# Performance work log

Measured on AMD Instinct MI355X. Metric: run time of the kernel, lower is better.

Reference implementation:

```python
import jax, jax.numpy as jnp
import numpy as np

B, N, D = 4, 2048, 512   # batch, seq, feed_forward_size
H, DK, DV = 8, 64, 64    # heads, key_dim, value_dim
LN_EPS = 1e-5


def setup_inputs() -> dict:
    key = jax.random.key(0)
    ks = jax.random.split(key, 12)
    s = 0.02
    x = jax.random.normal(ks[0], (B, N, D), dtype=jnp.float32)
    # boolean mask, True = masked out (torch masked_fill semantics); causal
    attn_mask = ~jnp.tril(jnp.ones((N, N), dtype=bool))[None, None]
    ln_g = jnp.ones((D,), jnp.float32)
    ln_b = jnp.zeros((D,), jnp.float32)
    wq = jax.random.normal(ks[1], (D, H * DK), jnp.float32) * s
    bq = jnp.zeros((H * DK,), jnp.float32)
    wk = jax.random.normal(ks[2], (D, H * DK), jnp.float32) * s
    bk = jnp.zeros((H * DK,), jnp.float32)
    wv = jax.random.normal(ks[3], (D, H * DV), jnp.float32) * s
    bv = jnp.zeros((H * DV,), jnp.float32)
    wo = jax.random.normal(ks[4], (H * DV, D), jnp.float32) * s
    bo = jnp.zeros((D,), jnp.float32)
    return {"x": x, "attn_mask": attn_mask, "ln_g": ln_g, "ln_b": ln_b,
            "wq": wq, "bq": bq, "wk": wk, "bk": bk, "wv": wv, "bv": bv,
            "wo": wo, "bo": bo}


def _layernorm(x, g, b):
    mu = jnp.mean(x, axis=-1, keepdims=True)
    var = jnp.mean(jnp.square(x - mu), axis=-1, keepdims=True)
    return (x - mu) * jax.lax.rsqrt(var + LN_EPS) * g + b


def reference(x, attn_mask, ln_g, ln_b, wq, bq, wk, bk, wv, bv, wo, bo):
    xn = _layernorm(x, ln_g, ln_b)
    scale = DK ** -0.5
    q = (xn @ wq + bq).reshape(B, N, H, DK).transpose(0, 2, 1, 3) * scale  # b h n d
    k = (xn @ wk + bk).reshape(B, N, H, DK).transpose(0, 2, 1, 3)
    v = (xn @ wv + bv).reshape(B, N, H, DV).transpose(0, 2, 1, 3)
    sim = jnp.einsum('bhid,bhjd->bhij', q, k)
    sim = jnp.where(attn_mask, -jnp.finfo(sim.dtype).max, sim)
    attn = jax.nn.softmax(sim, axis=-1)  # dropout p=0 (eval)
    out = jnp.einsum('bhij,bhjd->bhid', attn, v)
    out = out.transpose(0, 2, 1, 3).reshape(B, N, H * DV)  # b n (h d)
    return out @ wo + bo
```

## Files before the change

kernel.cpp:

```cpp
#include <hip/hip_runtime.h>

typedef unsigned short u16;
typedef unsigned long long u64;
typedef __bf16 bf16x8 __attribute__((ext_vector_type(8)));
typedef float f32x4 __attribute__((ext_vector_type(4)));
typedef float f32x16 __attribute__((ext_vector_type(16)));

#define H_HEADS 8
#define DHEAD 64
#define NSEQ 2048
#define DMODEL 512
#define BATCH 4
#define MROWS (BATCH * NSEQ)
#define BH (BATCH * H_HEADS)

__device__ __forceinline__ u16 f2bf(float f) {
  unsigned u = __builtin_bit_cast(unsigned, f);
  u += 0x7fffu + ((u >> 16) & 1u);
  return (u16)(u >> 16);
}

__device__ __forceinline__ float bf2f(u16 v) {
  unsigned u = (unsigned)v << 16;
  return __builtin_bit_cast(float, u);
}

__device__ __forceinline__ bf16x8 ldfrag(const u16* p) {
  return __builtin_bit_cast(bf16x8, *(const uint4*)p);
}

typedef __attribute__((address_space(1))) void GV;
typedef __attribute__((address_space(3))) void LV;
__device__ __forceinline__ void gld16(const void* g, void* l) {
  __builtin_amdgcn_global_load_lds((GV*)g, (LV*)l, 16, 0, 0);
}

__global__ __launch_bounds__(256) void ln_w_kernel(
    const float* __restrict__ x, const float* __restrict__ g,
    const float* __restrict__ b, u16* __restrict__ xn,
    const float* __restrict__ w0, const float* __restrict__ w1,
    const float* __restrict__ w2, const float* __restrict__ w3,
    u16* __restrict__ WT) {
  __shared__ float tile[32][33];
  const int t = threadIdx.x;
  if (blockIdx.x < MROWS) {
    const int row = blockIdx.x;
    const float2 v = *(const float2*)(x + (size_t)row * DMODEL + t * 2);
    float s = v.x + v.y;
    float ss = v.x * v.x + v.y * v.y;
    #pragma unroll
    for (int d = 1; d < 64; d <<= 1) {
      s += __shfl_xor(s, d);
      ss += __shfl_xor(ss, d);
    }
    const int wave = t >> 6, lane = t & 63;
    if (lane == 0) { tile[0][wave] = s; tile[0][4 + wave] = ss; }
    __syncthreads();
    s = tile[0][0] + tile[0][1] + tile[0][2] + tile[0][3];
    ss = tile[0][4] + tile[0][5] + tile[0][6] + tile[0][7];
    const float mean = s * (1.0f / DMODEL);
    const float var = ss * (1.0f / DMODEL) - mean * mean;
    const float rstd = rsqrtf(var + 1e-5f);
    const float2 gg = *(const float2*)(g + t * 2);
    const float2 bb = *(const float2*)(b + t * 2);
    const float o0 = (v.x - mean) * rstd * gg.x + bb.x;
    const float o1 = (v.y - mean) * rstd * gg.y + bb.y;
    const unsigned packed = (unsigned)f2bf(o0) | ((unsigned)f2bf(o1) << 16);
    *(unsigned*)(xn + (size_t)row * DMODEL + t * 2) = packed;
  } else {
    const int u = blockIdx.x - MROWS;
    const int z = u >> 8;
    const int rem = u & 255;
    const float* W = (z == 0) ? w0 : (z == 1) ? w1 : (z == 2) ? w2 : w3;
    u16* dst = WT + (size_t)z * DMODEL * DMODEL;
    const int n0 = (rem & 15) * 32, k0 = (rem >> 4) * 32;
    #pragma unroll
    for (int p = 0; p < 4; ++p) {
      const int uu = p * 256 + t;
      const int r = uu >> 5, c = uu & 31;
      tile[r][c] = W[(size_t)(k0 + r) * DMODEL + n0 + c];
    }
    __syncthreads();
    #pragma unroll
    for (int p = 0; p < 4; ++p) {
      const int uu = p * 256 + t;
      const int rn = uu >> 5, ck = uu & 31;
      dst[(size_t)(n0 + rn) * DMODEL + k0 + ck] = f2bf(tile[ck][rn]);
    }
  }
}

template <int MODE>
__global__ __launch_bounds__(512) void gemm128_kernel(
    const u16* __restrict__ A, const u16* __restrict__ BT,
    const float* __restrict__ bq, const float* __restrict__ bk,
    const float* __restrict__ bv,
    u16* __restrict__ qb, u16* __restrict__ kb, u16* __restrict__ vtb,
    float* __restrict__ fout, int K) {
  __shared__ u16 lds_a[128 * 64];
  __shared__ u16 lds_b[128 * 64];
  const int t = threadIdx.x;
  const int lane = t & 63, wave = t >> 6;
  const int wm = wave >> 2, wn = wave & 3;
  const int lo = lane & 15, hi = lane >> 4;
  const int nwg = gridDim.x * gridDim.y;
  const int lid = blockIdx.y * gridDim.x + blockIdx.x;
  const int sid = (lid & 7) * (nwg >> 3) + (lid >> 3);
  const int m0 = (sid / gridDim.x) * 128, n0 = (sid % gridDim.x) * 128;
  const int sr = lane >> 3;
  const int scol = (((lane & 7) ^ sr) * 8);
  f32x4 acc[4][2] = {};
  for (int k0 = 0; k0 < K; k0 += 64) {
    #pragma unroll
    for (int j = 0; j < 2; ++j) {
      const int ch = wave * 2 + j;
      gld16(A + (size_t)(m0 + ch * 8 + sr) * K + k0 + scol, lds_a + ch * 512);
      gld16(BT + (size_t)(n0 + ch * 8 + sr) * K + k0 + scol, lds_b + ch * 512);
    }
    __syncthreads();
    #pragma unroll
    for (int kc = 0; kc < 2; ++kc) {
      bf16x8 af[4], bfr[2];
      const int sw = ((lo & 7) * 8);
      #pragma unroll
      for (int i = 0; i < 4; ++i)
        af[i] = ldfrag(lds_a + (wm * 64 + i * 16 + lo) * 64 + ((kc * 32 + hi * 8) ^ sw));
      #pragma unroll
      for (int i = 0; i < 2; ++i)
        bfr[i] = ldfrag(lds_b + (wn * 32 + i * 16 + lo) * 64 + ((kc * 32 + hi * 8) ^ sw));
      __builtin_amdgcn_s_setprio(1);
      #pragma unroll
      for (int mi = 0; mi < 4; ++mi)
        #pragma unroll
        for (int ni = 0; ni < 2; ++ni)
          acc[mi][ni] = __builtin_amdgcn_mfma_f32_16x16x32_bf16(
              af[mi], bfr[ni], acc[mi][ni], 0, 0, 0);
      __builtin_amdgcn_s_setprio(0);
    }
    __syncthreads();
  }
  #pragma unroll
  for (int mi = 0; mi < 4; ++mi) {
    #pragma unroll
    for (int ni = 0; ni < 2; ++ni) {
      const int col = n0 + wn * 32 + ni * 16 + lo;
      if (MODE == 0) {
        const int mat = col >> 9, w = col & 511;
        const int hh = w >> 6, dk = w & 63;
        const float bi = (mat == 0 ? bq : (mat == 1 ? bk : bv))[w];
        const int row0 = m0 + wm * 64 + mi * 16 + hi * 4;
        const int bbx = row0 >> 11, seq0 = row0 & 2047;
        if (mat == 2) {
          u64 pk = 0;
          #pragma unroll
          for (int r = 0; r < 4; ++r)
            pk |= (u64)f2bf(acc[mi][ni][r] + bi) << (16 * r);
          *(u64*)(vtb + ((size_t)(bbx * H_HEADS + hh) * DHEAD + dk) * NSEQ + seq0) = pk;
        } else {
          const float sc = (mat == 0) ? 0.18033688f : 1.0f;
          u16* dst = (mat == 0 ? qb : kb);
          #pragma unroll
          for (int r = 0; r < 4; ++r)
            dst[(((size_t)(bbx * H_HEADS + hh) * NSEQ) + seq0 + r) * DHEAD + dk] =
                f2bf((acc[mi][ni][r] + bi) * sc);
        }
      } else {
        const float bi = bq[col];
        #pragma unroll
        for (int r = 0; r < 4; ++r) {
          const int row = m0 + wm * 64 + mi * 16 + hi * 4 + r;
          fout[(size_t)row * DMODEL + col] = acc[mi][ni][r] + bi;
        }
      }
    }
  }
}

__global__ __launch_bounds__(256, 4) void attn_kernel(
    const u16* __restrict__ Q, const u16* __restrict__ K,
    const u16* __restrict__ VT, u16* __restrict__ O,
    u16* __restrict__ pO, float* __restrict__ pL) {
  __shared__ u16 lds_k[2][4096];
  __shared__ u16 lds_v[2][4096];
  const int t = threadIdx.x;
  const int lane = t & 63, wave = t >> 6;
  const int l31 = lane & 31, hi = lane >> 5;
  const int l7 = lane & 7;

  const int nraw = blockIdx.x;
  const int n = (nraw & 7) * 160 + (nraw >> 3);
  const int bh = n / 40;
  const int r = n % 40;
  int qt, ck, C;
  if (r < 4)       { qt = r;                 C = 1; ck = 0; }
  else if (r < 12) { qt = 4 + ((r - 4) >> 1);  C = 2; ck = (r - 4) & 1; }
  else if (r < 24) { qt = 8 + (r - 12) / 3;    C = 3; ck = (r - 12) % 3; }
  else             { qt = 12 + ((r - 24) >> 2); C = 4; ck = (r - 24) & 3; }
  const int T = 2 * qt + 2;
  const int kc0 = (ck * T) / C;
  const int L = ((ck + 1) * T) / C - kc0;

  const int b = bh >> 3, h = bh & 7;
  const u16* Qh = Q + (size_t)bh * NSEQ * DHEAD;
  const u16* Kh = K + (size_t)bh * NSEQ * DHEAD;
  const u16* Vh = VT + (size_t)bh * DHEAD * NSEQ;

  const int q0w = qt * 128 + wave * 32;
  const int lastkt = (q0w + 31) >> 6;
  const int qrow = q0w + l31;

  bf16x8 qf[4];
  #pragma unroll
  for (int c = 0; c < 4; ++c)
    qf[c] = ldfrag(Qh + (size_t)qrow * DHEAD + c * 16 + hi * 8);

  f32x16 o0 = {}, o1 = {};
  float l = 0.0f;

  const int sr = lane >> 3;
  const int scol = ((lane & 7) ^ sr) * 8;
  const int swz = l7 * 8;

  #pragma unroll
  for (int j = 0; j < 2; ++j) {
    const int ch = wave * 2 + j;
    gld16(Kh + (size_t)(kc0 * 64 + ch * 8 + sr) * DHEAD + scol, lds_k[0] + ch * 512);
    gld16(Vh + (size_t)(ch * 8 + sr) * NSEQ + kc0 * 64 + scol, lds_v[0] + ch * 512);
  }

  for (int lt = 0; lt < L; ++lt) {
    const int gk = kc0 + lt;
    const int cur = lt & 1;
    if (lt + 1 < L) {
      const int kvn = (gk + 1) * 64;
      #pragma unroll
      for (int j = 0; j < 2; ++j) {
        const int ch = wave * 2 + j;
        gld16(Kh + (size_t)(kvn + ch * 8 + sr) * DHEAD + scol, lds_k[cur ^ 1] + ch * 512);
        gld16(Vh + (size_t)(ch * 8 + sr) * NSEQ + kvn + scol, lds_v[cur ^ 1] + ch * 512);
      }
      asm volatile("s_waitcnt vmcnt(4)" ::: "memory");
    } else {
      asm volatile("s_waitcnt vmcnt(0)" ::: "memory");
    }
    __builtin_amdgcn_s_barrier();
    __builtin_amdgcn_sched_barrier(0);

    if (gk <= lastkt) {
      const u16* lk = lds_k[cur];
      const u16* lv = lds_v[cur];
      f32x16 st0 = {}, st1 = {};

      __builtin_amdgcn_s_setprio(1);
      #pragma unroll
      for (int c = 0; c < 4; ++c) {
        const int col = (c * 16 + hi * 8) ^ swz;
        bf16x8 kf0 = ldfrag(lk + l31 * 64 + col);
        bf16x8 kf1 = ldfrag(lk + (32 + l31) * 64 + col);
        st0 = __builtin_amdgcn_mfma_f32_32x32x16_bf16(kf0, qf[c], st0, 0, 0, 0);
        st1 = __builtin_amdgcn_mfma_f32_32x32x16_bf16(kf1, qf[c], st1, 0, 0, 0);
      }
      __builtin_amdgcn_s_setprio(0);

      if (gk == lastkt) {
        const int kvb = gk * 64 + 4 * hi;
        #pragma unroll
        for (int rr = 0; rr < 16; ++rr) {
          const int kv = kvb + (rr & 3) + 8 * (rr >> 2);
          if (kv > qrow) st0[rr] = -1e30f;
          if (kv + 32 > qrow) st1[rr] = -1e30f;
        }
      }

      #pragma unroll
      for (int rr = 0; rr < 16; ++rr) st0[rr] = exp2f(st0[rr]);
      #pragma unroll
      for (int rr = 0; rr < 16; ++rr) st1[rr] = exp2f(st1[rr]);
      float sm[16];
      #pragma unroll
      for (int i = 0; i < 16; ++i) sm[i] = st0[i] + st1[i];
      #pragma unroll
      for (int stp = 8; stp; stp >>= 1)
        #pragma unroll
        for (int i = 0; i < stp; ++i) sm[i] += sm[i + stp];
      l += sm[0];

      bf16x8 pf0, pf1, pf2, pf3;
      {
        unsigned w0, w1, w2, w3, w4, w5, w6, w7;
        asm("v_cvt_pk_bf16_f32 %0, %1, %2" : "=v"(w0) : "v"(st0[0]), "v"(st0[1]));
        asm("v_cvt_pk_bf16_f32 %0, %1, %2" : "=v"(w1) : "v"(st0[2]), "v"(st0[3]));
        asm("v_cvt_pk_bf16_f32 %0, %1, %2" : "=v"(w2) : "v"(st0[4]), "v"(st0[5]));
        asm("v_cvt_pk_bf16_f32 %0, %1, %2" : "=v"(w3) : "v"(st0[6]), "v"(st0[7]));
        asm("v_cvt_pk_bf16_f32 %0, %1, %2" : "=v"(w4) : "v"(st0[8]), "v"(st0[9]));
        asm("v_cvt_pk_bf16_f32 %0, %1, %2" : "=v"(w5) : "v"(st0[10]), "v"(st0[11]));
        asm("v_cvt_pk_bf16_f32 %0, %1, %2" : "=v"(w6) : "v"(st0[12]), "v"(st0[13]));
        asm("v_cvt_pk_bf16_f32 %0, %1, %2" : "=v"(w7) : "v"(st0[14]), "v"(st0[15]));
        asm("v_permlane32_swap_b32 %0, %1" : "+v"(w0), "+v"(w2));
        asm("v_permlane32_swap_b32 %0, %1" : "+v"(w1), "+v"(w3));
        asm("v_permlane32_swap_b32 %0, %1" : "+v"(w4), "+v"(w6));
        asm("v_permlane32_swap_b32 %0, %1" : "+v"(w5), "+v"(w7));
        union Uu { unsigned u[4]; bf16x8 v; };
        Uu a; a.u[0] = w0; a.u[1] = w1; a.u[2] = w2; a.u[3] = w3; pf0 = a.v;
        Uu bb; bb.u[0] = w4; bb.u[1] = w5; bb.u[2] = w6; bb.u[3] = w7; pf1 = bb.v;
      }
      {
        unsigned w0, w1, w2, w3, w4, w5, w6, w7;
        asm("v_cvt_pk_bf16_f32 %0, %1, %2" : "=v"(w0) : "v"(st1[0]), "v"(st1[1]));
        asm("v_cvt_pk_bf16_f32 %0, %1, %2" : "=v"(w1) : "v"(st1[2]), "v"(st1[3]));
        asm("v_cvt_pk_bf16_f32 %0, %1, %2" : "=v"(w2) : "v"(st1[4]), "v"(st1[5]));
        asm("v_cvt_pk_bf16_f32 %0, %1, %2" : "=v"(w3) : "v"(st1[6]), "v"(st1[7]));
        asm("v_cvt_pk_bf16_f32 %0, %1, %2" : "=v"(w4) : "v"(st1[8]), "v"(st1[9]));
        asm("v_cvt_pk_bf16_f32 %0, %1, %2" : "=v"(w5) : "v"(st1[10]), "v"(st1[11]));
        asm("v_cvt_pk_bf16_f32 %0, %1, %2" : "=v"(w6) : "v"(st1[12]), "v"(st1[13]));
        asm("v_cvt_pk_bf16_f32 %0, %1, %2" : "=v"(w7) : "v"(st1[14]), "v"(st1[15]));
        asm("v_permlane32_swap_b32 %0, %1" : "+v"(w0), "+v"(w2));
        asm("v_permlane32_swap_b32 %0, %1" : "+v"(w1), "+v"(w3));
        asm("v_permlane32_swap_b32 %0, %1" : "+v"(w4), "+v"(w6));
        asm("v_permlane32_swap_b32 %0, %1" : "+v"(w5), "+v"(w7));
        union Uu { unsigned u[4]; bf16x8 v; };
        Uu a; a.u[0] = w0; a.u[1] = w1; a.u[2] = w2; a.u[3] = w3; pf2 = a.v;
        Uu bb; bb.u[0] = w4; bb.u[1] = w5; bb.u[2] = w6; bb.u[3] = w7; pf3 = bb.v;
      }

      __builtin_amdgcn_s_setprio(1);
      #pragma unroll
      for (int c = 0; c < 4; ++c) {
        const int col = (c * 16 + hi * 8) ^ swz;
        bf16x8 vf0 = ldfrag(lv + l31 * 64 + col);
        bf16x8 vf1 = ldfrag(lv + (32 + l31) * 64 + col);
        const bf16x8 pc = (c == 0) ? pf0 : (c == 1) ? pf1 : (c == 2) ? pf2 : pf3;
        o0 = __builtin_amdgcn_mfma_f32_32x32x16_bf16(vf0, pc, o0, 0, 0, 0);
        o1 = __builtin_amdgcn_mfma_f32_32x32x16_bf16(vf1, pc, o1, 0, 0, 0);
      }
      __builtin_amdgcn_s_setprio(0);
    }
    __builtin_amdgcn_sched_barrier(0);
    __builtin_amdgcn_s_barrier();
    __builtin_amdgcn_sched_barrier(0);
  }

  l += __shfl_xor(l, 32);

  if (C == 1) {
    const float rl = __builtin_amdgcn_rcpf(l);
    u16* Ob = O + ((size_t)b * NSEQ + qrow) * DMODEL + h * DHEAD;
    #pragma unroll
    for (int d = 0; d < 2; ++d) {
      #pragma unroll
      for (int mq = 0; mq < 4; ++mq) {
        u64 pk = 0;
        #pragma unroll
        for (int c3 = 0; c3 < 4; ++c3) {
          const float v = (d ? o1[mq * 4 + c3] : o0[mq * 4 + c3]) * rl;
          pk |= (u64)f2bf(v) << (16 * c3);
        }
        *(u64*)(Ob + d * 32 + mq * 8 + hi * 4) = pk;
      }
    }
  } else {
    const int rloc = wave * 32 + l31;
    u16* po = pO + (size_t)n * (128 * 64) + (size_t)rloc * 64;
    #pragma unroll
    for (int d = 0; d < 2; ++d) {
      #pragma unroll
      for (int mq = 0; mq < 4; ++mq) {
        u64 pk = 0;
        #pragma unroll
        for (int c3 = 0; c3 < 4; ++c3) {
          const float v = d ? o1[mq * 4 + c3] : o0[mq * 4 + c3];
          pk |= (u64)f2bf(v) << (16 * c3);
        }
        *(u64*)(po + d * 32 + mq * 8 + hi * 4) = pk;
      }
    }
    if (hi == 0) pL[(size_t)n * 128 + rloc] = l;
  }
}

__global__ __launch_bounds__(256) void attn_merge_kernel(
    const u16* __restrict__ pO, const float* __restrict__ pL,
    u16* __restrict__ O) {
  const int u = blockIdx.x;
  const int bh = u / 12, qi = u % 12;
  const int qt = 4 + qi;
  const int C = (qt >> 2) + 1;
  int off;
  if (qt < 8) off = 4 + 2 * (qt - 4);
  else if (qt < 12) off = 12 + 3 * (qt - 8);
  else off = 24 + 4 * (qt - 12);
  const int slot0 = bh * 40 + off;
  const int t = threadIdx.x;
  const int row = t >> 1, db = (t & 1) * 32;

  float ls = 0.0f;
  float a[32];
  #pragma unroll
  for (int k = 0; k < 32; ++k) a[k] = 0.0f;
  #pragma unroll
  for (int c = 0; c < 4; ++c) {
    if (c < C) {
      ls += pL[(size_t)(slot0 + c) * 128 + row];
      const u16* src = pO + (size_t)(slot0 + c) * (128 * 64) + (size_t)row * 64 + db;
      #pragma unroll
      for (int q4 = 0; q4 < 4; ++q4) {
        const uint4 v = *(const uint4*)(src + q4 * 8);
        const unsigned uu[4] = {v.x, v.y, v.z, v.w};
        #pragma unroll
        for (int j = 0; j < 4; ++j) {
          a[q4 * 8 + j * 2]     += bf2f((u16)(uu[j] & 0xffff));
          a[q4 * 8 + j * 2 + 1] += bf2f((u16)(uu[j] >> 16));
        }
      }
    }
  }
  const float rl = __builtin_amdgcn_rcpf(ls);
  const int b = bh >> 3, h = bh & 7;
  u16* dst = O + ((size_t)b * NSEQ + qt * 128 + row) * DMODEL + h * DHEAD + db;
  #pragma unroll
  for (int k4 = 0; k4 < 8; ++k4) {
    u64 pk = 0;
    #pragma unroll
    for (int j = 0; j < 4; ++j)
      pk |= (u64)f2bf(a[k4 * 4 + j] * rl) << (16 * j);
    *(u64*)(dst + k4 * 4) = pk;
  }
}

extern "C" void kernel_launch(void* const* d_in, const int* in_sizes, int n_in,
                              void* d_out, int out_size, void* d_ws, size_t ws_size,
                              hipStream_t stream) {
  const float* x = (const float*)d_in[0];
  const float* ln_g = (const float*)d_in[2];
  const float* ln_b = (const float*)d_in[3];
  const float* wq = (const float*)d_in[4];
  const float* bq = (const float*)d_in[5];
  const float* wk = (const float*)d_in[6];
  const float* bk = (const float*)d_in[7];
  const float* wv = (const float*)d_in[8];
  const float* bv = (const float*)d_in[9];
  const float* wo = (const float*)d_in[10];
  const float* bo = (const float*)d_in[11];

  char* ws = (char*)d_ws;
  u16* xn = (u16*)ws;     ws += (size_t)MROWS * DMODEL * 2;
  u16* wqkvT = (u16*)ws;  ws += (size_t)4 * DMODEL * DMODEL * 2;
  u16* woT = wqkvT + (size_t)3 * DMODEL * DMODEL;
  u16* qb = (u16*)ws;     ws += (size_t)MROWS * DMODEL * 2;
  u16* kb = (u16*)ws;     ws += (size_t)MROWS * DMODEL * 2;
  u16* vtb = (u16*)ws;    ws += (size_t)MROWS * DMODEL * 2;
  u16* attnb = (u16*)ws;  ws += (size_t)MROWS * DMODEL * 2;
  u16* pO = (u16*)ws;     ws += (size_t)1280 * 128 * 64 * 2;
  float* pL = (float*)ws; ws += (size_t)1280 * 128 * 4;

  ln_w_kernel<<<MROWS + 1024, 256, 0, stream>>>(
      x, ln_g, ln_b, xn, wq, wk, wv, wo, wqkvT);

  gemm128_kernel<0><<<dim3(12, 64), 512, 0, stream>>>(
      xn, wqkvT, bq, bk, bv, qb, kb, vtb, nullptr, DMODEL);

  attn_kernel<<<1280, 256, 0, stream>>>(qb, kb, vtb, attnb, pO, pL);
  attn_merge_kernel<<<384, 256, 0, stream>>>(pO, pL, attnb);

  gemm128_kernel<1><<<dim3(4, 64), 512, 0, stream>>>(
      attnb, woT, bo, nullptr, nullptr, nullptr, nullptr, nullptr,
      (float*)d_out, DMODEL);
}
```

Before: 95.64 us.

## Fuse split-KV attention merge into output projection GEMM A-tile load

The separate attention merge kernel and the attention output buffer are removed. The output-projection GEMM now builds its A tile by summing the split partial outputs, normalizing by the summed row sums, and writing bf16 into LDS. Every attention block, including single-chunk ones, now writes partials instead of the final output. This drops one launch and a full round trip of the attention output through global memory. In exchange, the merge work is repeated across the four N-tile blocks, and the A load becomes synchronous register loads instead of async global-to-LDS copies.

```diff
diff --git a/kernel.cpp b/kernel.cpp
--- a/kernel.cpp
+++ b/kernel.cpp
@@ -33,6 +33,13 @@
 typedef __attribute__((address_space(3))) void LV;
 __device__ __forceinline__ void gld16(const void* g, void* l) {
   __builtin_amdgcn_global_load_lds((GV*)g, (LV*)l, 16, 0, 0);
+}
+
+__device__ __forceinline__ int qt_off(int qt) {
+  if (qt < 4) return qt;
+  if (qt < 8) return 4 + 2 * (qt - 4);
+  if (qt < 12) return 12 + 3 * (qt - 8);
+  return 24 + 4 * (qt - 12);
 }
 
 __global__ __launch_bounds__(256) void ln_w_kernel(
@@ -90,32 +97,30 @@
   }
 }
 
-template <int MODE>
-__global__ __launch_bounds__(512) void gemm128_kernel(
+__global__ __launch_bounds__(512) void gemm_qkv_kernel(
     const u16* __restrict__ A, const u16* __restrict__ BT,
     const float* __restrict__ bq, const float* __restrict__ bk,
     const float* __restrict__ bv,
-    u16* __restrict__ qb, u16* __restrict__ kb, u16* __restrict__ vtb,
-    float* __restrict__ fout, int K) {
+    u16* __restrict__ qb, u16* __restrict__ kb, u16* __restrict__ vtb) {
   __shared__ u16 lds_a[128 * 64];
   __shared__ u16 lds_b[128 * 64];
   const int t = threadIdx.x;
   const int lane = t & 63, wave = t >> 6;
   const int wm = wave >> 2, wn = wave & 3;
   const int lo = lane & 15, hi = lane >> 4;
-  const int nwg = gridDim.x * gridDim.y;
-  const int lid = blockIdx.y * gridDim.x + blockIdx.x;
+  const int nwg = 12 * 64;
+  const int lid = blockIdx.y * 12 + blockIdx.x;
   const int sid = (lid & 7) * (nwg >> 3) + (lid >> 3);
-  const int m0 = (sid / gridDim.x) * 128, n0 = (sid % gridDim.x) * 128;
+  const int m0 = (sid / 12) * 128, n0 = (sid % 12) * 128;
   const int sr = lane >> 3;
   const int scol = (((lane & 7) ^ sr) * 8);
   f32x4 acc[4][2] = {};
-  for (int k0 = 0; k0 < K; k0 += 64) {
+  for (int k0 = 0; k0 < DMODEL; k0 += 64) {
     #pragma unroll
     for (int j = 0; j < 2; ++j) {
       const int ch = wave * 2 + j;
-      gld16(A + (size_t)(m0 + ch * 8 + sr) * K + k0 + scol, lds_a + ch * 512);
-      gld16(BT + (size_t)(n0 + ch * 8 + sr) * K + k0 + scol, lds_b + ch * 512);
+      gld16(A + (size_t)(m0 + ch * 8 + sr) * DMODEL + k0 + scol, lds_a + ch * 512);
+      gld16(BT + (size_t)(n0 + ch * 8 + sr) * DMODEL + k0 + scol, lds_b + ch * 512);
     }
     __syncthreads();
     #pragma unroll
@@ -144,33 +149,24 @@
     #pragma unroll
     for (int ni = 0; ni < 2; ++ni) {
       const int col = n0 + wn * 32 + ni * 16 + lo;
-      if (MODE == 0) {
-        const int mat = col >> 9, w = col & 511;
-        const int hh = w >> 6, dk = w & 63;
-        const float bi = (mat == 0 ? bq : (mat == 1 ? bk : bv))[w];
-        const int row0 = m0 + wm * 64 + mi * 16 + hi * 4;
-        const int bbx = row0 >> 11, seq0 = row0 & 2047;
-        if (mat == 2) {
-          u64 pk = 0;
-          #pragma unroll
-          for (int r = 0; r < 4; ++r)
-            pk |= (u64)f2bf(acc[mi][ni][r] + bi) << (16 * r);
-          *(u64*)(vtb + ((size_t)(bbx * H_HEADS + hh) * DHEAD + dk) * NSEQ + seq0) = pk;
-        } else {
-          const float sc = (mat == 0) ? 0.18033688f : 1.0f;
-          u16* dst = (mat == 0 ? qb : kb);
-          #pragma unroll
-          for (int r = 0; r < 4; ++r)
-            dst[(((size_t)(bbx * H_HEADS + hh) * NSEQ) + seq0 + r) * DHEAD + dk] =
-                f2bf((acc[mi][ni][r] + bi) * sc);
-        }
+      const int mat = col >> 9, w = col & 511;
+      const int hh = w >> 6, dk = w & 63;
+      const float bi = (mat == 0 ? bq : (mat == 1 ? bk : bv))[w];
+      const int row0 = m0 + wm * 64 + mi * 16 + hi * 4;
+      const int bbx = row0 >> 11, seq0 = row0 & 2047;
+      if (mat == 2) {
+        u64 pk = 0;
+        #pragma unroll
+        for (int r = 0; r < 4; ++r)
+          pk |= (u64)f2bf(acc[mi][ni][r] + bi) << (16 * r);
+        *(u64*)(vtb + ((size_t)(bbx * H_HEADS + hh) * DHEAD + dk) * NSEQ + seq0) = pk;
       } else {
-        const float bi = bq[col];
-        #pragma unroll
-        for (int r = 0; r < 4; ++r) {
-          const int row = m0 + wm * 64 + mi * 16 + hi * 4 + r;
-          fout[(size_t)row * DMODEL + col] = acc[mi][ni][r] + bi;
-        }
+        const float sc = (mat == 0) ? 0.18033688f : 1.0f;
+        u16* dst = (mat == 0 ? qb : kb);
+        #pragma unroll
+        for (int r = 0; r < 4; ++r)
+          dst[(((size_t)(bbx * H_HEADS + hh) * NSEQ) + seq0 + r) * DHEAD + dk] =
+              f2bf((acc[mi][ni][r] + bi) * sc);
       }
     }
   }
@@ -178,7 +174,7 @@
 
 __global__ __launch_bounds__(256, 4) void attn_kernel(
     const u16* __restrict__ Q, const u16* __restrict__ K,
-    const u16* __restrict__ VT, u16* __restrict__ O,
+    const u16* __restrict__ VT,
     u16* __restrict__ pO, float* __restrict__ pL) {
   __shared__ u16 lds_k[2][4096];
   __shared__ u16 lds_v[2][4096];
@@ -200,7 +196,6 @@
   const int kc0 = (ck * T) / C;
   const int L = ((ck + 1) * T) / C - kc0;
 
-  const int b = bh >> 3, h = bh & 7;
   const u16* Qh = Q + (size_t)bh * NSEQ * DHEAD;
   const u16* Kh = K + (size_t)bh * NSEQ * DHEAD;
   const u16* Vh = VT + (size_t)bh * DHEAD * NSEQ;
@@ -342,88 +337,111 @@
 
   l += __shfl_xor(l, 32);
 
-  if (C == 1) {
-    const float rl = __builtin_amdgcn_rcpf(l);
-    u16* Ob = O + ((size_t)b * NSEQ + qrow) * DMODEL + h * DHEAD;
-    #pragma unroll
-    for (int d = 0; d < 2; ++d) {
-      #pragma unroll
-      for (int mq = 0; mq < 4; ++mq) {
-        u64 pk = 0;
-        #pragma unroll
-        for (int c3 = 0; c3 < 4; ++c3) {
-          const float v = (d ? o1[mq * 4 + c3] : o0[mq * 4 + c3]) * rl;
-          pk |= (u64)f2bf(v) << (16 * c3);
-        }
-        *(u64*)(Ob + d * 32 + mq * 8 + hi * 4) = pk;
-      }
-    }
-  } else {
-    const int rloc = wave * 32 + l31;
-    u16* po = pO + (size_t)n * (128 * 64) + (size_t)rloc * 64;
-    #pragma unroll
-    for (int d = 0; d < 2; ++d) {
-      #pragma unroll
-      for (int mq = 0; mq < 4; ++mq) {
-        u64 pk = 0;
-        #pragma unroll
-        for (int c3 = 0; c3 < 4; ++c3) {
-          const float v = d ? o1[mq * 4 + c3] : o0[mq * 4 + c3];
-          pk |= (u64)f2bf(v) << (16 * c3);
-        }
-        *(u64*)(po + d * 32 + mq * 8 + hi * 4) = pk;
-      }
-    }
-    if (hi == 0) pL[(size_t)n * 128 + rloc] = l;
-  }
-}
-
-__global__ __launch_bounds__(256) void attn_merge_kernel(
+  const int rloc = wave * 32 + l31;
+  u16* po = pO + (size_t)n * (128 * 64) + (size_t)rloc * 64;
+  #pragma unroll
+  for (int d = 0; d < 2; ++d) {
+    #pragma unroll
+    for (int mq = 0; mq < 4; ++mq) {
+      u64 pk = 0;
+      #pragma unroll
+      for (int c3 = 0; c3 < 4; ++c3) {
+        const float v = d ? o1[mq * 4 + c3] : o0[mq * 4 + c3];
+        pk |= (u64)f2bf(v) << (16 * c3);
+      }
+      *(u64*)(po + d * 32 + mq * 8 + hi * 4) = pk;
+    }
+  }
+  if (hi == 0) pL[(size_t)n * 128 + rloc] = l;
+}
+
+__global__ __launch_bounds__(512) void gemm_out_kernel(
     const u16* __restrict__ pO, const float* __restrict__ pL,
-    u16* __restrict__ O) {
-  const int u = blockIdx.x;
-  const int bh = u / 12, qi = u % 12;
-  const int qt = 4 + qi;
+    const u16* __restrict__ BT, const float* __restrict__ bo,
+    float* __restrict__ fout) {
+  __shared__ u16 lds_a[128 * 64];
+  __shared__ u16 lds_b[128 * 64];
+  const int t = threadIdx.x;
+  const int lane = t & 63, wave = t >> 6;
+  const int wm = wave >> 2, wn = wave & 3;
+  const int lo = lane & 15, hi = lane >> 4;
+  const int nwg = 4 * 64;
+  const int lid = blockIdx.y * 4 + blockIdx.x;
+  const int sid = (lid & 7) * (nwg >> 3) + (lid >> 3);
+  const int m0 = (sid >> 2) * 128, n0 = (sid & 3) * 128;
+  const int sr = lane >> 3;
+  const int l7 = lane & 7;
+  const int scol = ((l7 ^ sr) * 8);
+
+  const int bq = m0 >> 11;
+  const int qt = (m0 & 2047) >> 7;
   const int C = (qt >> 2) + 1;
-  int off;
-  if (qt < 8) off = 4 + 2 * (qt - 4);
-  else if (qt < 12) off = 12 + 3 * (qt - 8);
-  else off = 24 + 4 * (qt - 12);
-  const int slot0 = bh * 40 + off;
-  const int t = threadIdx.x;
-  const int row = t >> 1, db = (t & 1) * 32;
-
-  float ls = 0.0f;
-  float a[32];
+  const int off = qt_off(qt);
+
+  f32x4 acc[4][2] = {};
+  for (int k0 = 0; k0 < DMODEL; k0 += 64) {
+    const int h = k0 >> 6;
+    const int slot0 = (bq * H_HEADS + h) * 40 + off;
+    #pragma unroll
+    for (int j = 0; j < 2; ++j) {
+      const int ch = wave * 2 + j;
+      const int row = ch * 8 + sr;
+      float ls = 0.0f;
+      float av[8] = {0.f, 0.f, 0.f, 0.f, 0.f, 0.f, 0.f, 0.f};
+      for (int c = 0; c < C; ++c) {
+        ls += pL[(size_t)(slot0 + c) * 128 + row];
+        const uint4 v = *(const uint4*)(pO + (size_t)(slot0 + c) * 8192 +
+                                        (size_t)row * 64 + l7 * 8);
+        const unsigned uu0 = v.x, uu1 = v.y, uu2 = v.z, uu3 = v.w;
+        av[0] += bf2f((u16)(uu0 & 0xffff)); av[1] += bf2f((u16)(uu0 >> 16));
+        av[2] += bf2f((u16)(uu1 & 0xffff)); av[3] += bf2f((u16)(uu1 >> 16));
+        av[4] += bf2f((u16)(uu2 & 0xffff)); av[5] += bf2f((u16)(uu2 >> 16));
+        av[6] += bf2f((u16)(uu3 & 0xffff)); av[7] += bf2f((u16)(uu3 >> 16));
+      }
+      const float rl = __builtin_amdgcn_rcpf(ls);
+      unsigned w0, w1, w2, w3;
+      asm("v_cvt_pk_bf16_f32 %0, %1, %2" : "=v"(w0) : "v"(av[0] * rl), "v"(av[1] * rl));
+      asm("v_cvt_pk_bf16_f32 %0, %1, %2" : "=v"(w1) : "v"(av[2] * rl), "v"(av[3] * rl));
+      asm("v_cvt_pk_bf16_f32 %0, %1, %2" : "=v"(w2) : "v"(av[4] * rl), "v"(av[5] * rl));
+      asm("v_cvt_pk_bf16_f32 %0, %1, %2" : "=v"(w3) : "v"(av[6] * rl), "v"(av[7] * rl));
+      uint4 pk; pk.x = w0; pk.y = w1; pk.z = w2; pk.w = w3;
+      *(uint4*)(lds_a + (size_t)row * 64 + scol) = pk;
+      gld16(BT + (size_t)(n0 + ch * 8 + sr) * DMODEL + k0 + scol, lds_b + ch * 512);
+    }
+    __syncthreads();
+    #pragma unroll
+    for (int kc = 0; kc < 2; ++kc) {
+      bf16x8 af[4], bfr[2];
+      const int sw = ((lo & 7) * 8);
+      #pragma unroll
+      for (int i = 0; i < 4; ++i)
+        af[i] = ldfrag(lds_a + (wm * 64 + i * 16 + lo) * 64 + ((kc * 32 + hi * 8) ^ sw));
+      #pragma unroll
+      for (int i = 0; i < 2; ++i)
+        bfr[i] = ldfrag(lds_b + (wn * 32 + i * 16 + lo) * 64 + ((kc * 32 + hi * 8) ^ sw));
+      __builtin_amdgcn_s_setprio(1);
+      #pragma unroll
+      for (int mi = 0; mi < 4; ++mi)
+        #pragma unroll
+        for (int ni = 0; ni < 2; ++ni)
+          acc[mi][ni] = __builtin_amdgcn_mfma_f32_16x16x32_bf16(
+              af[mi], bfr[ni], acc[mi][ni], 0, 0, 0);
+      __builtin_amdgcn_s_setprio(0);
+    }
+    __syncthreads();
+  }
   #pragma unroll
-  for (int k = 0; k < 32; ++k) a[k] = 0.0f;
-  #pragma unroll
-  for (int c = 0; c < 4; ++c) {
-    if (c < C) {
-      ls += pL[(size_t)(slot0 + c) * 128 + row];
-      const u16* src = pO + (size_t)(slot0 + c) * (128 * 64) + (size_t)row * 64 + db;
-      #pragma unroll
-      for (int q4 = 0; q4 < 4; ++q4) {
-        const uint4 v = *(const uint4*)(src + q4 * 8);
-        const unsigned uu[4] = {v.x, v.y, v.z, v.w};
-        #pragma unroll
-        for (int j = 0; j < 4; ++j) {
-          a[q4 * 8 + j * 2]     += bf2f((u16)(uu[j] & 0xffff));
-          a[q4 * 8 + j * 2 + 1] += bf2f((u16)(uu[j] >> 16));
-        }
-      }
-    }
-  }
-  const float rl = __builtin_amdgcn_rcpf(ls);
-  const int b = bh >> 3, h = bh & 7;
-  u16* dst = O + ((size_t)b * NSEQ + qt * 128 + row) * DMODEL + h * DHEAD + db;
-  #pragma unroll
-  for (int k4 = 0; k4 < 8; ++k4) {
-    u64 pk = 0;
-    #pragma unroll
-    for (int j = 0; j < 4; ++j)
-      pk |= (u64)f2bf(a[k4 * 4 + j] * rl) << (16 * j);
-    *(u64*)(dst + k4 * 4) = pk;
+  for (int mi = 0; mi < 4; ++mi) {
+    #pragma unroll
+    for (int ni = 0; ni < 2; ++ni) {
+      const int col = n0 + wn * 32 + ni * 16 + lo;
+      const float bi = bo[col];
+      #pragma unroll
+      for (int r = 0; r < 4; ++r) {
+        const int row = m0 + wm * 64 + mi * 16 + hi * 4 + r;
+        fout[(size_t)row * DMODEL + col] = acc[mi][ni][r] + bi;
+      }
+    }
   }
 }
 
@@ -449,20 +467,17 @@
   u16* qb = (u16*)ws;     ws += (size_t)MROWS * DMODEL * 2;
   u16* kb = (u16*)ws;     ws += (size_t)MROWS * DMODEL * 2;
   u16* vtb = (u16*)ws;    ws += (size_t)MROWS * DMODEL * 2;
-  u16* attnb = (u16*)ws;  ws += (size_t)MROWS * DMODEL * 2;
   u16* pO = (u16*)ws;     ws += (size_t)1280 * 128 * 64 * 2;
   float* pL = (float*)ws; ws += (size_t)1280 * 128 * 4;
 
   ln_w_kernel<<<MROWS + 1024, 256, 0, stream>>>(
       x, ln_g, ln_b, xn, wq, wk, wv, wo, wqkvT);
 
-  gemm128_kernel<0><<<dim3(12, 64), 512, 0, stream>>>(
-      xn, wqkvT, bq, bk, bv, qb, kb, vtb, nullptr, DMODEL);
-
-  attn_kernel<<<1280, 256, 0, stream>>>(qb, kb, vtb, attnb, pO, pL);
-  attn_merge_kernel<<<384, 256, 0, stream>>>(pO, pL, attnb);
-
-  gemm128_kernel<1><<<dim3(4, 64), 512, 0, stream>>>(
-      attnb, woT, bo, nullptr, nullptr, nullptr, nullptr, nullptr,
-      (float*)d_out, DMODEL);
-}
+  gemm_qkv_kernel<<<dim3(12, 64), 512, 0, stream>>>(
+      xn, wqkvT, bq, bk, bv, qb, kb, vtb);
+
+  attn_kernel<<<1280, 256, 0, stream>>>(qb, kb, vtb, pO, pL);
+
+  gemm_out_kernel<<<dim3(4, 64), 512, 0, stream>>>(
+      pO, pL, woT, bo, (float*)d_out);
+}
```

Result: slower. 104.6 us (+9.4%).

## Use 256-row query tiles with 512-thread attention blocks and fewer KV splits

Applied to the files above, without the earlier changes.

The attention kernel moves from 128-row query tiles with 4 waves to 256-row tiles with 8 waves, so each K/V tile staged in LDS is reused by twice as many query rows. The split-KV schedule shrinks from 40 to 20 chunks per head, which halves the block count and changes the partial-output layout and the merge indexing. The GEMM template is also split into two specialized kernels with compile-time grid constants. The larger blocks cut K/V load traffic but lower the number of concurrent blocks and may hurt load balance on the causal triangle.

```diff
diff --git a/kernel.cpp b/kernel.cpp
--- a/kernel.cpp
+++ b/kernel.cpp
@@ -13,6 +13,8 @@
 #define BATCH 4
 #define MROWS (BATCH * NSEQ)
 #define BH (BATCH * H_HEADS)
+#define NCHUNK 20
+#define NBLK (BH * NCHUNK)
 
 __device__ __forceinline__ u16 f2bf(float f) {
   unsigned u = __builtin_bit_cast(unsigned, f);
@@ -90,32 +92,30 @@
   }
 }
 
-template <int MODE>
-__global__ __launch_bounds__(512) void gemm128_kernel(
+__global__ __launch_bounds__(512) void gemm_qkv_kernel(
     const u16* __restrict__ A, const u16* __restrict__ BT,
     const float* __restrict__ bq, const float* __restrict__ bk,
     const float* __restrict__ bv,
-    u16* __restrict__ qb, u16* __restrict__ kb, u16* __restrict__ vtb,
-    float* __restrict__ fout, int K) {
+    u16* __restrict__ qb, u16* __restrict__ kb, u16* __restrict__ vtb) {
   __shared__ u16 lds_a[128 * 64];
   __shared__ u16 lds_b[128 * 64];
   const int t = threadIdx.x;
   const int lane = t & 63, wave = t >> 6;
   const int wm = wave >> 2, wn = wave & 3;
   const int lo = lane & 15, hi = lane >> 4;
-  const int nwg = gridDim.x * gridDim.y;
-  const int lid = blockIdx.y * gridDim.x + blockIdx.x;
+  const int nwg = 12 * 64;
+  const int lid = blockIdx.y * 12 + blockIdx.x;
   const int sid = (lid & 7) * (nwg >> 3) + (lid >> 3);
-  const int m0 = (sid / gridDim.x) * 128, n0 = (sid % gridDim.x) * 128;
+  const int m0 = (sid / 12) * 128, n0 = (sid % 12) * 128;
   const int sr = lane >> 3;
   const int scol = (((lane & 7) ^ sr) * 8);
   f32x4 acc[4][2] = {};
-  for (int k0 = 0; k0 < K; k0 += 64) {
+  for (int k0 = 0; k0 < DMODEL; k0 += 64) {
     #pragma unroll
     for (int j = 0; j < 2; ++j) {
       const int ch = wave * 2 + j;
-      gld16(A + (size_t)(m0 + ch * 8 + sr) * K + k0 + scol, lds_a + ch * 512);
-      gld16(BT + (size_t)(n0 + ch * 8 + sr) * K + k0 + scol, lds_b + ch * 512);
+      gld16(A + (size_t)(m0 + ch * 8 + sr) * DMODEL + k0 + scol, lds_a + ch * 512);
+      gld16(BT + (size_t)(n0 + ch * 8 + sr) * DMODEL + k0 + scol, lds_b + ch * 512);
     }
     __syncthreads();
     #pragma unroll
@@ -144,39 +144,30 @@
     #pragma unroll
     for (int ni = 0; ni < 2; ++ni) {
       const int col = n0 + wn * 32 + ni * 16 + lo;
-      if (MODE == 0) {
-        const int mat = col >> 9, w = col & 511;
-        const int hh = w >> 6, dk = w & 63;
-        const float bi = (mat == 0 ? bq : (mat == 1 ? bk : bv))[w];
-        const int row0 = m0 + wm * 64 + mi * 16 + hi * 4;
-        const int bbx = row0 >> 11, seq0 = row0 & 2047;
-        if (mat == 2) {
-          u64 pk = 0;
-          #pragma unroll
-          for (int r = 0; r < 4; ++r)
-            pk |= (u64)f2bf(acc[mi][ni][r] + bi) << (16 * r);
-          *(u64*)(vtb + ((size_t)(bbx * H_HEADS + hh) * DHEAD + dk) * NSEQ + seq0) = pk;
-        } else {
-          const float sc = (mat == 0) ? 0.18033688f : 1.0f;
-          u16* dst = (mat == 0 ? qb : kb);
-          #pragma unroll
-          for (int r = 0; r < 4; ++r)
-            dst[(((size_t)(bbx * H_HEADS + hh) * NSEQ) + seq0 + r) * DHEAD + dk] =
-                f2bf((acc[mi][ni][r] + bi) * sc);
-        }
+      const int mat = col >> 9, w = col & 511;
+      const int hh = w >> 6, dk = w & 63;
+      const float bi = (mat == 0 ? bq : (mat == 1 ? bk : bv))[w];
+      const int row0 = m0 + wm * 64 + mi * 16 + hi * 4;
+      const int bbx = row0 >> 11, seq0 = row0 & 2047;
+      if (mat == 2) {
+        u64 pk = 0;
+        #pragma unroll
+        for (int r = 0; r < 4; ++r)
+          pk |= (u64)f2bf(acc[mi][ni][r] + bi) << (16 * r);
+        *(u64*)(vtb + ((size_t)(bbx * H_HEADS + hh) * DHEAD + dk) * NSEQ + seq0) = pk;
       } else {
-        const float bi = bq[col];
-        #pragma unroll
-        for (int r = 0; r < 4; ++r) {
-          const int row = m0 + wm * 64 + mi * 16 + hi * 4 + r;
-          fout[(size_t)row * DMODEL + col] = acc[mi][ni][r] + bi;
-        }
-      }
-    }
-  }
-}
-
-__global__ __launch_bounds__(256, 4) void attn_kernel(
+        const float sc = (mat == 0) ? 0.18033688f : 1.0f;
+        u16* dst = (mat == 0 ? qb : kb);
+        #pragma unroll
+        for (int r = 0; r < 4; ++r)
+          dst[(((size_t)(bbx * H_HEADS + hh) * NSEQ) + seq0 + r) * DHEAD + dk] =
+              f2bf((acc[mi][ni][r] + bi) * sc);
+      }
+    }
+  }
+}
+
+__global__ __launch_bounds__(512, 4) void attn_kernel(
     const u16* __restrict__ Q, const u16* __restrict__ K,
     const u16* __restrict__ VT, u16* __restrict__ O,
     u16* __restrict__ pO, float* __restrict__ pL) {
@@ -188,15 +179,15 @@
   const int l7 = lane & 7;
 
   const int nraw = blockIdx.x;
-  const int n = (nraw & 7) * 160 + (nraw >> 3);
-  const int bh = n / 40;
-  const int r = n % 40;
+  const int n = (nraw & 7) * 80 + (nraw >> 3);
+  const int bh = n / NCHUNK;
+  const int r = n % NCHUNK;
   int qt, ck, C;
-  if (r < 4)       { qt = r;                 C = 1; ck = 0; }
-  else if (r < 12) { qt = 4 + ((r - 4) >> 1);  C = 2; ck = (r - 4) & 1; }
-  else if (r < 24) { qt = 8 + (r - 12) / 3;    C = 3; ck = (r - 12) % 3; }
-  else             { qt = 12 + ((r - 24) >> 2); C = 4; ck = (r - 24) & 3; }
-  const int T = 2 * qt + 2;
+  if (r < 2)       { qt = r;                  C = 1; ck = 0; }
+  else if (r < 6)  { qt = 2 + ((r - 2) >> 1); C = 2; ck = (r - 2) & 1; }
+  else if (r < 12) { qt = 4 + (r - 6) / 3;    C = 3; ck = (r - 6) % 3; }
+  else             { qt = 6 + ((r - 12) >> 2); C = 4; ck = (r - 12) & 3; }
+  const int T = 4 * qt + 4;
   const int kc0 = (ck * T) / C;
   const int L = ((ck + 1) * T) / C - kc0;
 
@@ -205,7 +196,7 @@
   const u16* Kh = K + (size_t)bh * NSEQ * DHEAD;
   const u16* Vh = VT + (size_t)bh * DHEAD * NSEQ;
 
-  const int q0w = qt * 128 + wave * 32;
+  const int q0w = qt * 256 + wave * 32;
   const int lastkt = (q0w + 31) >> 6;
   const int qrow = q0w + l31;
 
@@ -221,25 +212,17 @@
   const int scol = ((lane & 7) ^ sr) * 8;
   const int swz = l7 * 8;
 
-  #pragma unroll
-  for (int j = 0; j < 2; ++j) {
-    const int ch = wave * 2 + j;
-    gld16(Kh + (size_t)(kc0 * 64 + ch * 8 + sr) * DHEAD + scol, lds_k[0] + ch * 512);
-    gld16(Vh + (size_t)(ch * 8 + sr) * NSEQ + kc0 * 64 + scol, lds_v[0] + ch * 512);
-  }
+  gld16(Kh + (size_t)(kc0 * 64 + wave * 8 + sr) * DHEAD + scol, lds_k[0] + wave * 512);
+  gld16(Vh + (size_t)(wave * 8 + sr) * NSEQ + kc0 * 64 + scol, lds_v[0] + wave * 512);
 
   for (int lt = 0; lt < L; ++lt) {
     const int gk = kc0 + lt;
     const int cur = lt & 1;
     if (lt + 1 < L) {
       const int kvn = (gk + 1) * 64;
-      #pragma unroll
-      for (int j = 0; j < 2; ++j) {
-        const int ch = wave * 2 + j;
-        gld16(Kh + (size_t)(kvn + ch * 8 + sr) * DHEAD + scol, lds_k[cur ^ 1] + ch * 512);
-        gld16(Vh + (size_t)(ch * 8 + sr) * NSEQ + kvn + scol, lds_v[cur ^ 1] + ch * 512);
-      }
-      asm volatile("s_waitcnt vmcnt(4)" ::: "memory");
+      gld16(Kh + (size_t)(kvn + wave * 8 + sr) * DHEAD + scol, lds_k[cur ^ 1] + wave * 512);
+      gld16(Vh + (size_t)(wave * 8 + sr) * NSEQ + kvn + scol, lds_v[cur ^ 1] + wave * 512);
+      asm volatile("s_waitcnt vmcnt(2)" ::: "memory");
     } else {
       asm volatile("s_waitcnt vmcnt(0)" ::: "memory");
     }
@@ -360,7 +343,7 @@
     }
   } else {
     const int rloc = wave * 32 + l31;
-    u16* po = pO + (size_t)n * (128 * 64) + (size_t)rloc * 64;
+    u16* po = pO + (size_t)n * (256 * 64) + (size_t)rloc * 64;
     #pragma unroll
     for (int d = 0; d < 2; ++d) {
       #pragma unroll
@@ -374,7 +357,7 @@
         *(u64*)(po + d * 32 + mq * 8 + hi * 4) = pk;
       }
     }
-    if (hi == 0) pL[(size_t)n * 128 + rloc] = l;
+    if (hi == 0) pL[(size_t)n * 256 + rloc] = l;
   }
 }
 
@@ -382,16 +365,20 @@
     const u16* __restrict__ pO, const float* __restrict__ pL,
     u16* __restrict__ O) {
   const int u = blockIdx.x;
-  const int bh = u / 12, qi = u % 12;
-  const int qt = 4 + qi;
-  const int C = (qt >> 2) + 1;
+  const int bh = u / 12;
+  const int rem = u % 12;
+  const int qi = rem >> 1, rh = rem & 1;
+  const int qt = 2 + qi;
+  const int C = (qt >> 1) + 1;
   int off;
-  if (qt < 8) off = 4 + 2 * (qt - 4);
-  else if (qt < 12) off = 12 + 3 * (qt - 8);
-  else off = 24 + 4 * (qt - 12);
-  const int slot0 = bh * 40 + off;
+  switch (qi) {
+    case 0: off = 2; break;  case 1: off = 4; break;
+    case 2: off = 6; break;  case 3: off = 9; break;
+    case 4: off = 12; break; default: off = 16; break;
+  }
+  const int slot0 = bh * NCHUNK + off;
   const int t = threadIdx.x;
-  const int row = t >> 1, db = (t & 1) * 32;
+  const int row = rh * 128 + (t >> 1), db = (t & 1) * 32;
 
   float ls = 0.0f;
   float a[32];
@@ -400,8 +387,8 @@
   #pragma unroll
   for (int c = 0; c < 4; ++c) {
     if (c < C) {
-      ls += pL[(size_t)(slot0 + c) * 128 + row];
-      const u16* src = pO + (size_t)(slot0 + c) * (128 * 64) + (size_t)row * 64 + db;
+      ls += pL[(size_t)(slot0 + c) * 256 + row];
+      const u16* src = pO + (size_t)(slot0 + c) * (256 * 64) + (size_t)row * 64 + db;
       #pragma unroll
       for (int q4 = 0; q4 < 4; ++q4) {
         const uint4 v = *(const uint4*)(src + q4 * 8);
@@ -416,7 +403,7 @@
   }
   const float rl = __builtin_amdgcn_rcpf(ls);
   const int b = bh >> 3, h = bh & 7;
-  u16* dst = O + ((size_t)b * NSEQ + qt * 128 + row) * DMODEL + h * DHEAD + db;
+  u16* dst = O + ((size_t)b * NSEQ + qt * 256 + row) * DMODEL + h * DHEAD + db;
   #pragma unroll
   for (int k4 = 0; k4 < 8; ++k4) {
     u64 pk = 0;
@@ -424,6 +411,66 @@
     for (int j = 0; j < 4; ++j)
       pk |= (u64)f2bf(a[k4 * 4 + j] * rl) << (16 * j);
     *(u64*)(dst + k4 * 4) = pk;
+  }
+}
+
+__global__ __launch_bounds__(512) void gemm_out_kernel(
+    const u16* __restrict__ A, const u16* __restrict__ BT,
+    const float* __restrict__ bo, float* __restrict__ fout) {
+  __shared__ u16 lds_a[128 * 64];
+  __shared__ u16 lds_b[128 * 64];
+  const int t = threadIdx.x;
+  const int lane = t & 63, wave = t >> 6;
+  const int wm = wave >> 2, wn = wave & 3;
+  const int lo = lane & 15, hi = lane >> 4;
+  const int nwg = 4 * 64;
+  const int lid = blockIdx.y * 4 + blockIdx.x;
+  const int sid = (lid & 7) * (nwg >> 3) + (lid >> 3);
+  const int m0 = (sid >> 2) * 128, n0 = (sid & 3) * 128;
+  const int sr = lane >> 3;
+  const int scol = (((lane & 7) ^ sr) * 8);
+  f32x4 acc[4][2] = {};
+  for (int k0 = 0; k0 < DMODEL; k0 += 64) {
+    #pragma unroll
+    for (int j = 0; j < 2; ++j) {
+      const int ch = wave * 2 + j;
+      gld16(A + (size_t)(m0 + ch * 8 + sr) * DMODEL + k0 + scol, lds_a + ch * 512);
+      gld16(BT + (size_t)(n0 + ch * 8 + sr) * DMODEL + k0 + scol, lds_b + ch * 512);
+    }
+    __syncthreads();
+    #pragma unroll
+    for (int kc = 0; kc < 2; ++kc) {
+      bf16x8 af[4], bfr[2];
+      const int sw = ((lo & 7) * 8);
+      #pragma unroll
+      for (int i = 0; i < 4; ++i)
+        af[i] = ldfrag(lds_a + (wm * 64 + i * 16 + lo) * 64 + ((kc * 32 + hi * 8) ^ sw));
+      #pragma unroll
+      for (int i = 0; i < 2; ++i)
+        bfr[i] = ldfrag(lds_b + (wn * 32 + i * 16 + lo) * 64 + ((kc * 32 + hi * 8) ^ sw));
+      __builtin_amdgcn_s_setprio(1);
+      #pragma unroll
+      for (int mi = 0; mi < 4; ++mi)
+        #pragma unroll
+        for (int ni = 0; ni < 2; ++ni)
+          acc[mi][ni] = __builtin_amdgcn_mfma_f32_16x16x32_bf16(
+              af[mi], bfr[ni], acc[mi][ni], 0, 0, 0);
+      __builtin_amdgcn_s_setprio(0);
+    }
+    __syncthreads();
+  }
+  #pragma unroll
+  for (int mi = 0; mi < 4; ++mi) {
+    #pragma unroll
+    for (int ni = 0; ni < 2; ++ni) {
+      const int col = n0 + wn * 32 + ni * 16 + lo;
+      const float bi = bo[col];
+      #pragma unroll
+      for (int r = 0; r < 4; ++r) {
+        const int row = m0 + wm * 64 + mi * 16 + hi * 4 + r;
+        fout[(size_t)row * DMODEL + col] = acc[mi][ni][r] + bi;
+      }
+    }
   }
 }
 
@@ -450,19 +497,18 @@
   u16* kb = (u16*)ws;     ws += (size_t)MROWS * DMODEL * 2;
   u16* vtb = (u16*)ws;    ws += (size_t)MROWS * DMODEL * 2;
   u16* attnb = (u16*)ws;  ws += (size_t)MROWS * DMODEL * 2;
-  u16* pO = (u16*)ws;     ws += (size_t)1280 * 128 * 64 * 2;
-  float* pL = (float*)ws; ws += (size_t)1280 * 128 * 4;
+  u16* pO = (u16*)ws;     ws += (size_t)NBLK * 256 * 64 * 2;
+  float* pL = (float*)ws; ws += (size_t)NBLK * 256 * 4;
 
   ln_w_kernel<<<MROWS + 1024, 256, 0, stream>>>(
       x, ln_g, ln_b, xn, wq, wk, wv, wo, wqkvT);
 
-  gemm128_kernel<0><<<dim3(12, 64), 512, 0, stream>>>(
-      xn, wqkvT, bq, bk, bv, qb, kb, vtb, nullptr, DMODEL);
-
-  attn_kernel<<<1280, 256, 0, stream>>>(qb, kb, vtb, attnb, pO, pL);
-  attn_merge_kernel<<<384, 256, 0, stream>>>(pO, pL, attnb);
-
-  gemm128_kernel<1><<<dim3(4, 64), 512, 0, stream>>>(
-      attnb, woT, bo, nullptr, nullptr, nullptr, nullptr, nullptr,
-      (float*)d_out, DMODEL);
-}
+  gemm_qkv_kernel<<<dim3(12, 64), 512, 0, stream>>>(
+      xn, wqkvT, bq, bk, bv, qb, kb, vtb);
+
+  attn_kernel<<<NBLK, 512, 0, stream>>>(qb, kb, vtb, attnb, pO, pL);
+  attn_merge_kernel<<<32 * 12, 256, 0, stream>>>(pO, pL, attnb);
+
+  gemm_out_kernel<<<dim3(4, 64), 512, 0, stream>>>(
+      attnb, woT, bo, (float*)d_out);
+}
```

Measured after the change: 97.86 us. 2.3% more time.

## Double-buffer LDS tiles in GEMM to overlap global loads with MFMA

Applied to the files above, without the earlier changes.

Splits the GEMM's A and B shared-memory tiles into two buffers. The next K-slice is prefetched with direct global-to-LDS loads while the current slice feeds the MFMAs, using explicit vmcnt waits and raw barriers in place of __syncthreads. This hides global load latency that the single-buffered loop exposed at each step. In exchange it doubles LDS use to 64KB per block, which can lower occupancy, and it depends on the hand-written waitcnt and barrier ordering being correct.

```diff
diff --git a/kernel.cpp b/kernel.cpp
--- a/kernel.cpp
+++ b/kernel.cpp
@@ -97,8 +97,8 @@
     const float* __restrict__ bv,
     u16* __restrict__ qb, u16* __restrict__ kb, u16* __restrict__ vtb,
     float* __restrict__ fout, int K) {
-  __shared__ u16 lds_a[128 * 64];
-  __shared__ u16 lds_b[128 * 64];
+  __shared__ u16 lds_a[2][128 * 64];
+  __shared__ u16 lds_b[2][128 * 64];
   const int t = threadIdx.x;
   const int lane = t & 63, wave = t >> 6;
   const int wm = wave >> 2, wn = wave & 3;
@@ -110,24 +110,42 @@
   const int sr = lane >> 3;
   const int scol = (((lane & 7) ^ sr) * 8);
   f32x4 acc[4][2] = {};
-  for (int k0 = 0; k0 < K; k0 += 64) {
-    #pragma unroll
-    for (int j = 0; j < 2; ++j) {
-      const int ch = wave * 2 + j;
-      gld16(A + (size_t)(m0 + ch * 8 + sr) * K + k0 + scol, lds_a + ch * 512);
-      gld16(BT + (size_t)(n0 + ch * 8 + sr) * K + k0 + scol, lds_b + ch * 512);
-    }
-    __syncthreads();
+  const int nk = K >> 6;
+
+  #pragma unroll
+  for (int j = 0; j < 2; ++j) {
+    const int ch = wave * 2 + j;
+    gld16(A + (size_t)(m0 + ch * 8 + sr) * K + scol, lds_a[0] + ch * 512);
+    gld16(BT + (size_t)(n0 + ch * 8 + sr) * K + scol, lds_b[0] + ch * 512);
+  }
+
+  for (int k = 0; k < nk; ++k) {
+    const int cur = k & 1;
+    if (k + 1 < nk) {
+      const int k0 = (k + 1) << 6;
+      #pragma unroll
+      for (int j = 0; j < 2; ++j) {
+        const int ch = wave * 2 + j;
+        gld16(A + (size_t)(m0 + ch * 8 + sr) * K + k0 + scol, lds_a[cur ^ 1] + ch * 512);
+        gld16(BT + (size_t)(n0 + ch * 8 + sr) * K + k0 + scol, lds_b[cur ^ 1] + ch * 512);
+      }
+      asm volatile("s_waitcnt vmcnt(4)" ::: "memory");
+    } else {
+      asm volatile("s_waitcnt vmcnt(0)" ::: "memory");
+    }
+    __builtin_amdgcn_s_barrier();
+    __builtin_amdgcn_sched_barrier(0);
+
     #pragma unroll
     for (int kc = 0; kc < 2; ++kc) {
       bf16x8 af[4], bfr[2];
       const int sw = ((lo & 7) * 8);
       #pragma unroll
       for (int i = 0; i < 4; ++i)
-        af[i] = ldfrag(lds_a + (wm * 64 + i * 16 + lo) * 64 + ((kc * 32 + hi * 8) ^ sw));
+        af[i] = ldfrag(lds_a[cur] + (wm * 64 + i * 16 + lo) * 64 + ((kc * 32 + hi * 8) ^ sw));
       #pragma unroll
       for (int i = 0; i < 2; ++i)
-        bfr[i] = ldfrag(lds_b + (wn * 32 + i * 16 + lo) * 64 + ((kc * 32 + hi * 8) ^ sw));
+        bfr[i] = ldfrag(lds_b[cur] + (wn * 32 + i * 16 + lo) * 64 + ((kc * 32 + hi * 8) ^ sw));
       __builtin_amdgcn_s_setprio(1);
       #pragma unroll
       for (int mi = 0; mi < 4; ++mi)
@@ -137,8 +155,11 @@
               af[mi], bfr[ni], acc[mi][ni], 0, 0, 0);
       __builtin_amdgcn_s_setprio(0);
     }
-    __syncthreads();
-  }
+    __builtin_amdgcn_sched_barrier(0);
+    __builtin_amdgcn_s_barrier();
+    __builtin_amdgcn_sched_barrier(0);
+  }
+
   #pragma unroll
   for (int mi = 0; mi < 4; ++mi) {
     #pragma unroll
```

Result: no change. 95.04 us, median of 2 (-0.6%).
